# Kernel optimization log

Measured on AMD Instinct MI355X. Metric: run time of the kernel, lower is better.

Reference implementation:

```python
import jax, jax.numpy as jnp
import numpy as np

NUM_ROUTING = 3


def squash(s, axis=-1):
    # squash(s) = |s|^2/(1+|s|^2) * s/|s|  (no epsilon, matching the torch code)
    sq = jnp.sum(s * s, axis=axis, keepdims=True)
    return sq / (1.0 + sq) * (s / jnp.sqrt(sq))


def setup_inputs() -> dict:
    key = jax.random.key(0)
    k1, k2 = jax.random.split(key)
    B, in_dim, in_num = 256, 8, 1152
    out_num, out_dim = 10, 16
    x = jax.random.normal(k1, (B, in_dim, in_num), dtype=jnp.float32)
    W = jax.random.normal(k2, (in_num, out_num, out_dim, in_dim), dtype=jnp.float32)
    return {"x": x, "W": W}


def reference(x, W):
    # x: [B, in_dim, in_num]; W: [in_num(i), out_num(j), out_dim(d), in_dim(c)]
    B = x.shape[0]
    in_num, out_num = W.shape[0], W.shape[1]
    # u_hat[i,j,b,d] = sum_c W[i,j,d,c] * x[b,c,i]
    u_hat = jnp.einsum('ijdc,bci->ijbd', W, x)
    b_ij = jnp.zeros((in_num, out_num), dtype=x.dtype)
    v = None
    for _ in range(NUM_ROUTING):
        # DGL reduce: softmax over the output-capsule axis (bucket dim)
        c = jax.nn.softmax(b_ij, axis=1)                    # [i, j]
        s = jnp.einsum('ij,ijbd->jbd', c, u_hat)            # [j, B, d]
        v = squash(s, axis=2)                               # [j, B, d]
        # edge update: b_ij += mean_b sum_d v[j,b,d] * u_hat[i,j,b,d]
        b_ij = b_ij + jnp.einsum('jbd,ijbd->ij', v, u_hat) / B
    # output: [B, out_num, out_dim, 1]
    return jnp.transpose(v, (1, 0, 2))[..., None]
```

## Files before the change

kernel.cpp:

```cpp
#include <hip/hip_runtime.h>

#define IN_NUM 1152
#define OUT_NUM 10
#define OUT_DIM 16
#define IN_DIM 8
#define NB 256
#define KTOT 9216

#define OFF_SPART 0
#define SZ_SPART (96 * OUT_NUM * OUT_DIM * NB)
#define OFF_VT (OFF_SPART + SZ_SPART)
#define SZ_VT (NB * OUT_NUM * OUT_DIM)
#define OFF_BP (OFF_VT + SZ_VT)
#define SZ_BP (32 * IN_NUM * OUT_NUM)
#define OFF_WT (OFF_BP + SZ_BP)
#define SZ_WT (OUT_NUM * OUT_DIM * IN_DIM * IN_NUM)

#define SMEM_FLOATS 5792

__device__ __forceinline__ void phase0(float* smem, int t, int w,
                                       const float* __restrict__ W, float* __restrict__ Wt) {
    float (*lds)[129] = (float (*)[129])smem;
    int r0 = t >> 5, c4 = t & 31;
    int itile = w / 10, j = w - itile * 10;
    int i0 = itile * 32;
#pragma unroll
    for (int rr = 0; rr < 4; ++rr) {
        int r = rr * 8 + r0;
        float4 w4 = *reinterpret_cast<const float4*>(
            &W[(size_t)(i0 + r) * 1280 + j * 128 + c4 * 4]);
        lds[r][c4 * 4 + 0] = w4.x; lds[r][c4 * 4 + 1] = w4.y;
        lds[r][c4 * 4 + 2] = w4.z; lds[r][c4 * 4 + 3] = w4.w;
    }
    __syncthreads();
    int ii = t & 31, dcq = t >> 5;
#pragma unroll
    for (int rr = 0; rr < 16; ++rr) {
        int dc = rr * 8 + dcq;
        Wt[(size_t)(j * 128 + dc) * IN_NUM + i0 + ii] = lds[ii][dc];
    }
}

__device__ __forceinline__ void phase1(float* smem, int t, int w, int it,
                                       const float* __restrict__ x, const float* __restrict__ Wt,
                                       const float* __restrict__ bp, float* __restrict__ spart) {
    int g8 = w / 80, r = w - g8 * 80;
    int j = r >> 3, isp = g8 * 8 + (r & 7);
    int cch = isp / 12;
    int i0 = (isp - cch * 12) * 96;
    int k0 = isp * 96;
    float (*xt)[260] = (float (*)[260])smem;
    float (*at)[16]  = (float (*)[16])(smem + 4160);
    float* ldc = smem + 5696;
    if (t < 96) {
        float cv;
        if (it == 0) {
            cv = 0.1f;
        } else {
            int i = i0 + t;
            float bt_[OUT_NUM];
#pragma unroll
            for (int jp = 0; jp < OUT_NUM; ++jp) bt_[jp] = 0.f;
#pragma unroll
            for (int row = 0; row < 32; ++row) {
                const float* p = &bp[((size_t)row * IN_NUM + i) * OUT_NUM];
#pragma unroll
                for (int jp = 0; jp < OUT_NUM; ++jp) bt_[jp] += p[jp];
            }
            float m = -1e30f;
#pragma unroll
            for (int jp = 0; jp < OUT_NUM; ++jp) { bt_[jp] *= (1.f / NB); m = fmaxf(m, bt_[jp]); }
            float s = 0.f;
#pragma unroll
            for (int jp = 0; jp < OUT_NUM; ++jp) { bt_[jp] = __expf(bt_[jp] - m); s += bt_[jp]; }
            cv = bt_[j] / s;
        }
        ldc[t] = cv;
    }
    __syncthreads();
    for (int e = t; e < 1536; e += 256) {
        int d = e / 96, kk = e - d * 96;
        at[kk][d] = ldc[kk] * Wt[(size_t)(j * 16 + d) * KTOT + cch * IN_NUM + i0 + kk];
    }
    int bb = t & 63, dg = t >> 6;
    int q4 = t & 3, row = t >> 2;
    float acc[16];
#pragma unroll
    for (int q = 0; q < 16; ++q) acc[q] = 0.f;
    for (int ch = 0; ch < 6; ++ch) {
        __syncthreads();
#pragma unroll
        for (int rr = 0; rr < 4; ++rr) {
            int b = rr * 64 + row;
            float4 xv = *reinterpret_cast<const float4*>(
                &x[(size_t)b * KTOT + k0 + ch * 16 + q4 * 4]);
            xt[q4 * 4 + 0][b] = xv.x; xt[q4 * 4 + 1][b] = xv.y;
            xt[q4 * 4 + 2][b] = xv.z; xt[q4 * 4 + 3][b] = xv.w;
        }
        __syncthreads();
#pragma unroll
        for (int kk = 0; kk < 16; ++kk) {
            float4 xv = *reinterpret_cast<const float4*>(&xt[kk][bb * 4]);
            float4 a4 = *reinterpret_cast<const float4*>(&at[ch * 16 + kk][dg * 4]);
            acc[0]  += a4.x * xv.x; acc[1]  += a4.x * xv.y; acc[2]  += a4.x * xv.z; acc[3]  += a4.x * xv.w;
            acc[4]  += a4.y * xv.x; acc[5]  += a4.y * xv.y; acc[6]  += a4.y * xv.z; acc[7]  += a4.y * xv.w;
            acc[8]  += a4.z * xv.x; acc[9]  += a4.z * xv.y; acc[10] += a4.z * xv.z; acc[11] += a4.z * xv.w;
            acc[12] += a4.w * xv.x; acc[13] += a4.w * xv.y; acc[14] += a4.w * xv.z; acc[15] += a4.w * xv.w;
        }
    }
    float* sp = spart + (size_t)(isp * OUT_NUM + j) * (OUT_DIM * NB);
#pragma unroll
    for (int dd = 0; dd < 4; ++dd) {
        float4 o;
        o.x = acc[dd * 4 + 0]; o.y = acc[dd * 4 + 1];
        o.z = acc[dd * 4 + 2]; o.w = acc[dd * 4 + 3];
        *reinterpret_cast<float4*>(&sp[(dg * 4 + dd) * NB + bb * 4]) = o;
    }
}

__device__ __forceinline__ void phase2(float* smem, int t, int w,
                                       const float* __restrict__ spart, float* __restrict__ dst) {
    float (*red)[32][17] = (float (*)[32][17])smem;
    float (*nrm)[9] = (float (*)[9])(smem + 4352);
    float* cf = smem + 4640;
    int j = w >> 3, bt2 = w & 7;
    int ie = t >> 5, bb = t & 31;
    int b = bt2 * 32 + bb;
    float acc[16];
#pragma unroll
    for (int d = 0; d < 16; ++d) acc[d] = 0.f;
    for (int q = 0; q < 12; ++q) {
        int isp = ie * 12 + q;
        const float* sp = spart + (size_t)(isp * OUT_NUM + j) * (OUT_DIM * NB) + b;
#pragma unroll
        for (int d = 0; d < 16; ++d) acc[d] += sp[d * NB];
    }
#pragma unroll
    for (int d = 0; d < 16; ++d) red[ie][bb][d] = acc[d];
    __syncthreads();
    int bb2 = t >> 3, dp = t & 7;
    float s0 = 0.f, s1 = 0.f;
#pragma unroll
    for (int e = 0; e < 8; ++e) { s0 += red[e][bb2][dp * 2]; s1 += red[e][bb2][dp * 2 + 1]; }
    nrm[bb2][dp] = s0 * s0 + s1 * s1;
    __syncthreads();
    if (t < 32) {
        float qn = 0.f;
#pragma unroll
        for (int d = 0; d < 8; ++d) qn += nrm[t][d];
        cf[t] = qn / ((1.f + qn) * sqrtf(qn));
    }
    __syncthreads();
    float cs = cf[bb2];
    float* o = dst + (size_t)(bt2 * 32 + bb2) * (OUT_NUM * OUT_DIM) + j * OUT_DIM + dp * 2;
    o[0] = s0 * cs;
    o[1] = s1 * cs;
}

__device__ __forceinline__ void phase3(int u, int t, int it,
                                       const float* __restrict__ x, const float* __restrict__ vt,
                                       const float* __restrict__ Wt, float* __restrict__ bp) {
    int kt = u % 36;
    int jq = u / 36;
    int j = jq >> 2, bq = jq & 3;
    int k = kt * 256 + t;
    int c = k / IN_NUM, i = k - c * IN_NUM;
    const float* xk = x + k + (size_t)(bq * 64) * KTOT;
    const float* vjb = vt + (size_t)(bq * 64) * (OUT_NUM * OUT_DIM) + j * OUT_DIM;
    float macc[16];
#pragma unroll
    for (int d = 0; d < 16; ++d) macc[d] = 0.f;
#pragma unroll 8
    for (int b = 0; b < 64; ++b) {
        float xv = xk[(size_t)b * KTOT];
        const float* vb = vjb + (size_t)b * (OUT_NUM * OUT_DIM);
#pragma unroll
        for (int d = 0; d < 16; ++d) macc[d] += vb[d] * xv;
    }
    float bs = 0.f;
#pragma unroll
    for (int d = 0; d < 16; ++d)
        bs += macc[d] * Wt[(size_t)(j * OUT_DIM + d) * KTOT + k];
    size_t idx = (size_t)(bq * 8 + c) * (IN_NUM * OUT_NUM) + (size_t)i * OUT_NUM + j;
    float prev = (it == 0) ? 0.f : bp[idx];
    bp[idx] = prev + bs;
}

__global__ __launch_bounds__(256, 4) void k_p0(const float* __restrict__ W, float* __restrict__ ws) {
    __shared__ float smem[SMEM_FLOATS];
    phase0(smem, threadIdx.x, blockIdx.x, W, ws + OFF_WT);
}
__global__ __launch_bounds__(256, 4) void k_p1(const float* __restrict__ x, float* __restrict__ ws, int it) {
    __shared__ float smem[SMEM_FLOATS];
    phase1(smem, threadIdx.x, blockIdx.x, it, x, ws + OFF_WT, ws + OFF_BP, ws + OFF_SPART);
}
__global__ __launch_bounds__(256, 4) void k_p2(const float* __restrict__ ws, float* __restrict__ dst) {
    __shared__ float smem[SMEM_FLOATS];
    phase2(smem, threadIdx.x, blockIdx.x, ws + OFF_SPART, dst);
}
__global__ __launch_bounds__(256) void k_p3(const float* __restrict__ x, float* __restrict__ ws, int it) {
    phase3(blockIdx.x, threadIdx.x, it, x, ws + OFF_VT, ws + OFF_WT, ws + OFF_BP);
}

extern "C" void kernel_launch(void* const* d_in, const int* in_sizes, int n_in,
                              void* d_out, int out_size, void* d_ws, size_t ws_size,
                              hipStream_t stream) {
    const float* x = (const float*)d_in[0];
    const float* W = (const float*)d_in[1];
    float* out = (float*)d_out;
    float* ws = (float*)d_ws;

    k_p0<<<dim3(360), dim3(256), 0, stream>>>(W, ws);
    for (int it = 0; it < 3; ++it) {
        k_p1<<<dim3(960), dim3(256), 0, stream>>>(x, ws, it);
        k_p2<<<dim3(80), dim3(256), 0, stream>>>(ws, it == 2 ? out : (ws + OFF_VT));
        if (it < 2) k_p3<<<dim3(1440), dim3(256), 0, stream>>>(x, ws, it);
    }
}
```

Measured before the change: 122.5 us.

## Fuse W transpose into first routing GEMM and double per-thread d tile

Removes the separate W transpose kernel: on the first routing iteration, phase1 reads raw W with a strided gather, writes the transposed copy to the workspace for later iterations, and uses it directly with the uniform coefficient. Phase1 blocks also shrink to 128 threads, each computing 8 output dims by 4 batch entries (32 accumulators) instead of 4x4. This saves one launch and an extra pass over W, and gives more register reuse per LDS load. In exchange the first iteration does uncoalesced W reads and writes, there are fewer threads per block, and register pressure is higher.

```diff
diff --git a/kernel.cpp b/kernel.cpp
--- a/kernel.cpp
+++ b/kernel.cpp
@@ -18,31 +18,9 @@
 
 #define SMEM_FLOATS 5792
 
-__device__ __forceinline__ void phase0(float* smem, int t, int w,
-                                       const float* __restrict__ W, float* __restrict__ Wt) {
-    float (*lds)[129] = (float (*)[129])smem;
-    int r0 = t >> 5, c4 = t & 31;
-    int itile = w / 10, j = w - itile * 10;
-    int i0 = itile * 32;
-#pragma unroll
-    for (int rr = 0; rr < 4; ++rr) {
-        int r = rr * 8 + r0;
-        float4 w4 = *reinterpret_cast<const float4*>(
-            &W[(size_t)(i0 + r) * 1280 + j * 128 + c4 * 4]);
-        lds[r][c4 * 4 + 0] = w4.x; lds[r][c4 * 4 + 1] = w4.y;
-        lds[r][c4 * 4 + 2] = w4.z; lds[r][c4 * 4 + 3] = w4.w;
-    }
-    __syncthreads();
-    int ii = t & 31, dcq = t >> 5;
-#pragma unroll
-    for (int rr = 0; rr < 16; ++rr) {
-        int dc = rr * 8 + dcq;
-        Wt[(size_t)(j * 128 + dc) * IN_NUM + i0 + ii] = lds[ii][dc];
-    }
-}
-
 __device__ __forceinline__ void phase1(float* smem, int t, int w, int it,
-                                       const float* __restrict__ x, const float* __restrict__ Wt,
+                                       const float* __restrict__ x, const float* __restrict__ W,
+                                       float* __restrict__ Wt,
                                        const float* __restrict__ bp, float* __restrict__ spart) {
     int g8 = w / 80, r = w - g8 * 80;
     int j = r >> 3, isp = g8 * 8 + (r & 7);
@@ -78,20 +56,29 @@
         ldc[t] = cv;
     }
     __syncthreads();
-    for (int e = t; e < 1536; e += 256) {
-        int d = e / 96, kk = e - d * 96;
-        at[kk][d] = ldc[kk] * Wt[(size_t)(j * 16 + d) * KTOT + cch * IN_NUM + i0 + kk];
+    if (it == 0) {
+        for (int e = t; e < 1536; e += 128) {
+            int d = e / 96, kk = e - d * 96;
+            float raw = W[(size_t)(i0 + kk) * 1280 + j * 128 + d * 8 + cch];
+            Wt[(size_t)(j * 16 + d) * KTOT + cch * IN_NUM + i0 + kk] = raw;
+            at[kk][d] = 0.1f * raw;
+        }
+    } else {
+        for (int e = t; e < 1536; e += 128) {
+            int d = e / 96, kk = e - d * 96;
+            at[kk][d] = ldc[kk] * Wt[(size_t)(j * 16 + d) * KTOT + cch * IN_NUM + i0 + kk];
+        }
     }
     int bb = t & 63, dg = t >> 6;
     int q4 = t & 3, row = t >> 2;
-    float acc[16];
-#pragma unroll
-    for (int q = 0; q < 16; ++q) acc[q] = 0.f;
+    float acc[32];
+#pragma unroll
+    for (int q = 0; q < 32; ++q) acc[q] = 0.f;
     for (int ch = 0; ch < 6; ++ch) {
         __syncthreads();
 #pragma unroll
-        for (int rr = 0; rr < 4; ++rr) {
-            int b = rr * 64 + row;
+        for (int rr = 0; rr < 8; ++rr) {
+            int b = rr * 32 + row;
             float4 xv = *reinterpret_cast<const float4*>(
                 &x[(size_t)b * KTOT + k0 + ch * 16 + q4 * 4]);
             xt[q4 * 4 + 0][b] = xv.x; xt[q4 * 4 + 1][b] = xv.y;
@@ -101,20 +88,25 @@
 #pragma unroll
         for (int kk = 0; kk < 16; ++kk) {
             float4 xv = *reinterpret_cast<const float4*>(&xt[kk][bb * 4]);
-            float4 a4 = *reinterpret_cast<const float4*>(&at[ch * 16 + kk][dg * 4]);
-            acc[0]  += a4.x * xv.x; acc[1]  += a4.x * xv.y; acc[2]  += a4.x * xv.z; acc[3]  += a4.x * xv.w;
-            acc[4]  += a4.y * xv.x; acc[5]  += a4.y * xv.y; acc[6]  += a4.y * xv.z; acc[7]  += a4.y * xv.w;
-            acc[8]  += a4.z * xv.x; acc[9]  += a4.z * xv.y; acc[10] += a4.z * xv.z; acc[11] += a4.z * xv.w;
-            acc[12] += a4.w * xv.x; acc[13] += a4.w * xv.y; acc[14] += a4.w * xv.z; acc[15] += a4.w * xv.w;
+            float4 a0 = *reinterpret_cast<const float4*>(&at[ch * 16 + kk][dg * 8]);
+            float4 a1 = *reinterpret_cast<const float4*>(&at[ch * 16 + kk][dg * 8 + 4]);
+            acc[0]  += a0.x * xv.x; acc[1]  += a0.x * xv.y; acc[2]  += a0.x * xv.z; acc[3]  += a0.x * xv.w;
+            acc[4]  += a0.y * xv.x; acc[5]  += a0.y * xv.y; acc[6]  += a0.y * xv.z; acc[7]  += a0.y * xv.w;
+            acc[8]  += a0.z * xv.x; acc[9]  += a0.z * xv.y; acc[10] += a0.z * xv.z; acc[11] += a0.z * xv.w;
+            acc[12] += a0.w * xv.x; acc[13] += a0.w * xv.y; acc[14] += a0.w * xv.z; acc[15] += a0.w * xv.w;
+            acc[16] += a1.x * xv.x; acc[17] += a1.x * xv.y; acc[18] += a1.x * xv.z; acc[19] += a1.x * xv.w;
+            acc[20] += a1.y * xv.x; acc[21] += a1.y * xv.y; acc[22] += a1.y * xv.z; acc[23] += a1.y * xv.w;
+            acc[24] += a1.z * xv.x; acc[25] += a1.z * xv.y; acc[26] += a1.z * xv.z; acc[27] += a1.z * xv.w;
+            acc[28] += a1.w * xv.x; acc[29] += a1.w * xv.y; acc[30] += a1.w * xv.z; acc[31] += a1.w * xv.w;
         }
     }
     float* sp = spart + (size_t)(isp * OUT_NUM + j) * (OUT_DIM * NB);
 #pragma unroll
-    for (int dd = 0; dd < 4; ++dd) {
+    for (int dd = 0; dd < 8; ++dd) {
         float4 o;
         o.x = acc[dd * 4 + 0]; o.y = acc[dd * 4 + 1];
         o.z = acc[dd * 4 + 2]; o.w = acc[dd * 4 + 3];
-        *reinterpret_cast<float4*>(&sp[(dg * 4 + dd) * NB + bb * 4]) = o;
+        *reinterpret_cast<float4*>(&sp[(dg * 8 + dd) * NB + bb * 4]) = o;
     }
 }
 
@@ -186,13 +178,10 @@
     bp[idx] = prev + bs;
 }
 
-__global__ __launch_bounds__(256, 4) void k_p0(const float* __restrict__ W, float* __restrict__ ws) {
+__global__ __launch_bounds__(128, 4) void k_p1(const float* __restrict__ x, const float* __restrict__ W,
+                                               float* __restrict__ ws, int it) {
     __shared__ float smem[SMEM_FLOATS];
-    phase0(smem, threadIdx.x, blockIdx.x, W, ws + OFF_WT);
-}
-__global__ __launch_bounds__(256, 4) void k_p1(const float* __restrict__ x, float* __restrict__ ws, int it) {
-    __shared__ float smem[SMEM_FLOATS];
-    phase1(smem, threadIdx.x, blockIdx.x, it, x, ws + OFF_WT, ws + OFF_BP, ws + OFF_SPART);
+    phase1(smem, threadIdx.x, blockIdx.x, it, x, W, ws + OFF_WT, ws + OFF_BP, ws + OFF_SPART);
 }
 __global__ __launch_bounds__(256, 4) void k_p2(const float* __restrict__ ws, float* __restrict__ dst) {
     __shared__ float smem[SMEM_FLOATS];
@@ -210,9 +199,8 @@
     float* out = (float*)d_out;
     float* ws = (float*)d_ws;
 
-    k_p0<<<dim3(360), dim3(256), 0, stream>>>(W, ws);
     for (int it = 0; it < 3; ++it) {
-        k_p1<<<dim3(960), dim3(256), 0, stream>>>(x, ws, it);
+        k_p1<<<dim3(960), dim3(128), 0, stream>>>(x, W, ws, it);
         k_p2<<<dim3(80), dim3(256), 0, stream>>>(ws, it == 2 ? out : (ws + OFF_VT));
         if (it < 2) k_p3<<<dim3(1440), dim3(256), 0, stream>>>(x, ws, it);
     }
```

Measured after the change: 126.4 us. +3.1%, slower.

## Pre-transpose x and W into workspace so the routing GEMM runs without LDS

Applied to the files above, without the earlier changes.

A fused prep kernel now transposes x into a [k][b] layout and also writes a second W copy laid out as [j][k][d], alongside the existing transposed W. The phase-1 kernel drops its LDS staging and syncthreads: each thread owns one batch element, reads x with coalesced loads and broadcasts W rows, and accumulates 16 outputs. The per-input-capsule logit reduction now uses float2 loads. This costs an extra transpose of x and an extra copy of W in global memory each call, and phase 1 gives up register tiling over the batch dimension.

```diff
diff --git a/kernel.cpp b/kernel.cpp
--- a/kernel.cpp
+++ b/kernel.cpp
@@ -9,49 +9,94 @@
 
 #define OFF_SPART 0
 #define SZ_SPART (96 * OUT_NUM * OUT_DIM * NB)
-#define OFF_VT (OFF_SPART + SZ_SPART)
+#define OFF_BP (OFF_SPART + SZ_SPART)
+#define SZ_BP (32 * IN_NUM * OUT_NUM)
+#define OFF_VT (OFF_BP + SZ_BP)
 #define SZ_VT (NB * OUT_NUM * OUT_DIM)
-#define OFF_BP (OFF_VT + SZ_VT)
-#define SZ_BP (32 * IN_NUM * OUT_NUM)
-#define OFF_WT (OFF_BP + SZ_BP)
-#define SZ_WT (OUT_NUM * OUT_DIM * IN_DIM * IN_NUM)
-
-#define SMEM_FLOATS 5792
-
-__device__ __forceinline__ void phase0(float* smem, int t, int w,
-                                       const float* __restrict__ W, float* __restrict__ Wt) {
-    float (*lds)[129] = (float (*)[129])smem;
-    int r0 = t >> 5, c4 = t & 31;
-    int itile = w / 10, j = w - itile * 10;
-    int i0 = itile * 32;
-#pragma unroll
-    for (int rr = 0; rr < 4; ++rr) {
-        int r = rr * 8 + r0;
-        float4 w4 = *reinterpret_cast<const float4*>(
-            &W[(size_t)(i0 + r) * 1280 + j * 128 + c4 * 4]);
-        lds[r][c4 * 4 + 0] = w4.x; lds[r][c4 * 4 + 1] = w4.y;
-        lds[r][c4 * 4 + 2] = w4.z; lds[r][c4 * 4 + 3] = w4.w;
-    }
-    __syncthreads();
-    int ii = t & 31, dcq = t >> 5;
-#pragma unroll
-    for (int rr = 0; rr < 16; ++rr) {
-        int dc = rr * 8 + dcq;
-        Wt[(size_t)(j * 128 + dc) * IN_NUM + i0 + ii] = lds[ii][dc];
-    }
-}
-
-__device__ __forceinline__ void phase1(float* smem, int t, int w, int it,
-                                       const float* __restrict__ x, const float* __restrict__ Wt,
-                                       const float* __restrict__ bp, float* __restrict__ spart) {
+#define OFF_WT (OFF_VT + SZ_VT)
+#define SZ_WT (OUT_NUM * OUT_DIM * KTOT)
+#define OFF_WT2 (OFF_WT + SZ_WT)
+#define SZ_WT2 (OUT_NUM * KTOT * OUT_DIM)
+#define OFF_XT (OFF_WT2 + SZ_WT2)
+#define SZ_XT (KTOT * NB)
+
+__global__ __launch_bounds__(256) void k_prep(const float* __restrict__ x,
+                                              const float* __restrict__ W,
+                                              float* __restrict__ ws) {
+    __shared__ float smem[64 * 68];
+    float* xT = ws + OFF_XT;
+    float* Wt = ws + OFF_WT;
+    float* Wt2 = ws + OFF_WT2;
+    int u = blockIdx.x, t = threadIdx.x;
+    if (u < 576) {
+        float (*lds)[68] = (float (*)[68])smem;
+        int kt = u % 144, bt = u / 144;
+        int k0 = kt * 64, b0 = bt * 64;
+        int r = t >> 4, c4 = (t & 15) * 4;
+#pragma unroll
+        for (int p = 0; p < 4; ++p) {
+            int bb = p * 16 + r;
+            float4 v = *reinterpret_cast<const float4*>(&x[(size_t)(b0 + bb) * KTOT + k0 + c4]);
+            lds[bb][c4 + 0] = v.x; lds[bb][c4 + 1] = v.y;
+            lds[bb][c4 + 2] = v.z; lds[bb][c4 + 3] = v.w;
+        }
+        __syncthreads();
+#pragma unroll
+        for (int p = 0; p < 4; ++p) {
+            int kk = p * 16 + r;
+            float4 o;
+            o.x = lds[c4 + 0][kk]; o.y = lds[c4 + 1][kk];
+            o.z = lds[c4 + 2][kk]; o.w = lds[c4 + 3][kk];
+            *reinterpret_cast<float4*>(&xT[(size_t)(k0 + kk) * NB + b0 + c4]) = o;
+        }
+    } else {
+        float (*lds2)[129] = (float (*)[129])smem;
+        int w = u - 576;
+        int itile = w / 10, j = w - itile * 10;
+        int i0 = itile * 32;
+        int r0 = t >> 5, c4b = t & 31;
+#pragma unroll
+        for (int rr = 0; rr < 4; ++rr) {
+            int rrow = rr * 8 + r0;
+            float4 w4 = *reinterpret_cast<const float4*>(
+                &W[(size_t)(i0 + rrow) * 1280 + j * 128 + c4b * 4]);
+            lds2[rrow][c4b * 4 + 0] = w4.x; lds2[rrow][c4b * 4 + 1] = w4.y;
+            lds2[rrow][c4b * 4 + 2] = w4.z; lds2[rrow][c4b * 4 + 3] = w4.w;
+        }
+        __syncthreads();
+        int ii = t & 31, dcq = t >> 5;
+#pragma unroll
+        for (int rr = 0; rr < 16; ++rr) {
+            int dc = rr * 8 + dcq;
+            Wt[(size_t)(j * 128 + dc) * IN_NUM + i0 + ii] = lds2[ii][dc];
+        }
+        int d4 = t & 3, ii2 = (t >> 2) & 31, ch0 = t >> 7;
+#pragma unroll
+        for (int c2 = 0; c2 < 4; ++c2) {
+            int c = c2 * 2 + ch0;
+            float4 o;
+            o.x = lds2[ii2][(d4 * 4 + 0) * 8 + c];
+            o.y = lds2[ii2][(d4 * 4 + 1) * 8 + c];
+            o.z = lds2[ii2][(d4 * 4 + 2) * 8 + c];
+            o.w = lds2[ii2][(d4 * 4 + 3) * 8 + c];
+            *reinterpret_cast<float4*>(
+                &Wt2[((size_t)j * KTOT + c * IN_NUM + i0 + ii2) * OUT_DIM + d4 * 4]) = o;
+        }
+    }
+}
+
+__global__ __launch_bounds__(256, 4) void k_p1(float* __restrict__ ws, int it) {
+    __shared__ float ldc[96];
+    const float* xT = ws + OFF_XT;
+    const float* Wt2 = ws + OFF_WT2;
+    const float* bp = ws + OFF_BP;
+    float* spart = ws + OFF_SPART;
+    int w = blockIdx.x, t = threadIdx.x;
     int g8 = w / 80, r = w - g8 * 80;
     int j = r >> 3, isp = g8 * 8 + (r & 7);
     int cch = isp / 12;
     int i0 = (isp - cch * 12) * 96;
     int k0 = isp * 96;
-    float (*xt)[260] = (float (*)[260])smem;
-    float (*at)[16]  = (float (*)[16])(smem + 4160);
-    float* ldc = smem + 5696;
     if (t < 96) {
         float cv;
         if (it == 0) {
@@ -61,11 +106,15 @@
             float bt_[OUT_NUM];
 #pragma unroll
             for (int jp = 0; jp < OUT_NUM; ++jp) bt_[jp] = 0.f;
-#pragma unroll
+#pragma unroll 4
             for (int row = 0; row < 32; ++row) {
-                const float* p = &bp[((size_t)row * IN_NUM + i) * OUT_NUM];
-#pragma unroll
-                for (int jp = 0; jp < OUT_NUM; ++jp) bt_[jp] += p[jp];
+                const float2* p2 = reinterpret_cast<const float2*>(
+                    &bp[(size_t)row * (IN_NUM * OUT_NUM) + i * OUT_NUM]);
+#pragma unroll
+                for (int q = 0; q < 5; ++q) {
+                    float2 v = p2[q];
+                    bt_[q * 2] += v.x; bt_[q * 2 + 1] += v.y;
+                }
             }
             float m = -1e30f;
 #pragma unroll
@@ -78,52 +127,32 @@
         ldc[t] = cv;
     }
     __syncthreads();
-    for (int e = t; e < 1536; e += 256) {
-        int d = e / 96, kk = e - d * 96;
-        at[kk][d] = ldc[kk] * Wt[(size_t)(j * 16 + d) * KTOT + cch * IN_NUM + i0 + kk];
-    }
-    int bb = t & 63, dg = t >> 6;
-    int q4 = t & 3, row = t >> 2;
+    const float* xp = xT + (size_t)k0 * NB + t;
+    const float* wp = Wt2 + ((size_t)j * KTOT + k0) * OUT_DIM;
     float acc[16];
 #pragma unroll
-    for (int q = 0; q < 16; ++q) acc[q] = 0.f;
-    for (int ch = 0; ch < 6; ++ch) {
-        __syncthreads();
-#pragma unroll
-        for (int rr = 0; rr < 4; ++rr) {
-            int b = rr * 64 + row;
-            float4 xv = *reinterpret_cast<const float4*>(
-                &x[(size_t)b * KTOT + k0 + ch * 16 + q4 * 4]);
-            xt[q4 * 4 + 0][b] = xv.x; xt[q4 * 4 + 1][b] = xv.y;
-            xt[q4 * 4 + 2][b] = xv.z; xt[q4 * 4 + 3][b] = xv.w;
-        }
-        __syncthreads();
-#pragma unroll
-        for (int kk = 0; kk < 16; ++kk) {
-            float4 xv = *reinterpret_cast<const float4*>(&xt[kk][bb * 4]);
-            float4 a4 = *reinterpret_cast<const float4*>(&at[ch * 16 + kk][dg * 4]);
-            acc[0]  += a4.x * xv.x; acc[1]  += a4.x * xv.y; acc[2]  += a4.x * xv.z; acc[3]  += a4.x * xv.w;
-            acc[4]  += a4.y * xv.x; acc[5]  += a4.y * xv.y; acc[6]  += a4.y * xv.z; acc[7]  += a4.y * xv.w;
-            acc[8]  += a4.z * xv.x; acc[9]  += a4.z * xv.y; acc[10] += a4.z * xv.z; acc[11] += a4.z * xv.w;
-            acc[12] += a4.w * xv.x; acc[13] += a4.w * xv.y; acc[14] += a4.w * xv.z; acc[15] += a4.w * xv.w;
-        }
-    }
-    float* sp = spart + (size_t)(isp * OUT_NUM + j) * (OUT_DIM * NB);
-#pragma unroll
-    for (int dd = 0; dd < 4; ++dd) {
-        float4 o;
-        o.x = acc[dd * 4 + 0]; o.y = acc[dd * 4 + 1];
-        o.z = acc[dd * 4 + 2]; o.w = acc[dd * 4 + 3];
-        *reinterpret_cast<float4*>(&sp[(dg * 4 + dd) * NB + bb * 4]) = o;
-    }
-}
-
-__device__ __forceinline__ void phase2(float* smem, int t, int w,
-                                       const float* __restrict__ spart, float* __restrict__ dst) {
+    for (int d = 0; d < 16; ++d) acc[d] = 0.f;
+#pragma unroll 4
+    for (int kk = 0; kk < 96; ++kk) {
+        float xv = xp[(size_t)kk * NB];
+        float xs = xv * ldc[kk];
+        const float* a = wp + kk * OUT_DIM;
+#pragma unroll
+        for (int d = 0; d < 16; ++d) acc[d] += a[d] * xs;
+    }
+    float* sp = spart + ((size_t)isp * OUT_NUM + j) * (OUT_DIM * NB) + t;
+#pragma unroll
+    for (int d = 0; d < 16; ++d) sp[d * NB] = acc[d];
+}
+
+__global__ __launch_bounds__(256, 4) void k_p2(const float* __restrict__ ws, float* __restrict__ dst) {
+    __shared__ float smem[4672];
     float (*red)[32][17] = (float (*)[32][17])smem;
     float (*nrm)[9] = (float (*)[9])(smem + 4352);
     float* cf = smem + 4640;
-    int j = w >> 3, bt2 = w & 7;
+    const float* spart = ws + OFF_SPART;
+    int wvar = blockIdx.x, t = threadIdx.x;
+    int j = wvar >> 3, bt2 = wvar & 7;
     int ie = t >> 5, bb = t & 31;
     int b = bt2 * 32 + bb;
     float acc[16];
@@ -157,9 +186,12 @@
     o[1] = s1 * cs;
 }
 
-__device__ __forceinline__ void phase3(int u, int t, int it,
-                                       const float* __restrict__ x, const float* __restrict__ vt,
-                                       const float* __restrict__ Wt, float* __restrict__ bp) {
+__global__ __launch_bounds__(256) void k_p3(const float* __restrict__ x,
+                                            float* __restrict__ ws, int it) {
+    const float* vt = ws + OFF_VT;
+    const float* Wt = ws + OFF_WT;
+    float* bp = ws + OFF_BP;
+    int u = blockIdx.x, t = threadIdx.x;
     int kt = u % 36;
     int jq = u / 36;
     int j = jq >> 2, bq = jq & 3;
@@ -186,22 +218,6 @@
     bp[idx] = prev + bs;
 }
 
-__global__ __launch_bounds__(256, 4) void k_p0(const float* __restrict__ W, float* __restrict__ ws) {
-    __shared__ float smem[SMEM_FLOATS];
-    phase0(smem, threadIdx.x, blockIdx.x, W, ws + OFF_WT);
-}
-__global__ __launch_bounds__(256, 4) void k_p1(const float* __restrict__ x, float* __restrict__ ws, int it) {
-    __shared__ float smem[SMEM_FLOATS];
-    phase1(smem, threadIdx.x, blockIdx.x, it, x, ws + OFF_WT, ws + OFF_BP, ws + OFF_SPART);
-}
-__global__ __launch_bounds__(256, 4) void k_p2(const float* __restrict__ ws, float* __restrict__ dst) {
-    __shared__ float smem[SMEM_FLOATS];
-    phase2(smem, threadIdx.x, blockIdx.x, ws + OFF_SPART, dst);
-}
-__global__ __launch_bounds__(256) void k_p3(const float* __restrict__ x, float* __restrict__ ws, int it) {
-    phase3(blockIdx.x, threadIdx.x, it, x, ws + OFF_VT, ws + OFF_WT, ws + OFF_BP);
-}
-
 extern "C" void kernel_launch(void* const* d_in, const int* in_sizes, int n_in,
                               void* d_out, int out_size, void* d_ws, size_t ws_size,
                               hipStream_t stream) {
@@ -210,9 +226,9 @@
     float* out = (float*)d_out;
     float* ws = (float*)d_ws;
 
-    k_p0<<<dim3(360), dim3(256), 0, stream>>>(W, ws);
+    k_prep<<<dim3(936), dim3(256), 0, stream>>>(x, W, ws);
     for (int it = 0; it < 3; ++it) {
-        k_p1<<<dim3(960), dim3(256), 0, stream>>>(x, ws, it);
+        k_p1<<<dim3(960), dim3(256), 0, stream>>>(ws, it);
         k_p2<<<dim3(80), dim3(256), 0, stream>>>(ws, it == 2 ? out : (ws + OFF_VT));
         if (it < 2) k_p3<<<dim3(1440), dim3(256), 0, stream>>>(x, ws, it);
     }
```

After: 123.0 us. Within noise of the previous version (+0.4%).
